# Kernel tuning notes

Hardware: AMD Instinct MI355X
Metric: run time of the kernel (lower is better)

The kernel has to match this reference:

```python
import jax, jax.numpy as jnp
import numpy as np

B, T, I, H = 64, 512, 1024, 1024


def setup_inputs() -> dict:
    key = jax.random.key(0)
    k1, k2, k3, k4 = jax.random.split(key, 4)
    stdv = 1.0 / np.sqrt(H)
    x = jax.random.normal(k1, (B, T, I), dtype=jnp.float32)
    w_ih = jax.random.uniform(k2, (4 * H, I), minval=-stdv, maxval=stdv, dtype=jnp.float32)
    w_hh = jax.random.uniform(k3, (4 * H, H), minval=-stdv, maxval=stdv, dtype=jnp.float32)
    b = jax.random.uniform(k4, (4 * H,), minval=-stdv, maxval=stdv, dtype=jnp.float32)
    return {"x": x, "w_ih": w_ih, "w_hh": w_hh, "b": b}


def _lstm(x, w_ih, w_hh, b):
    # Precompute input projections for all timesteps: [T, B, 4H]
    xg = jnp.einsum('bti,gi->tbg', x, w_ih) + b

    def step(carry, xg_t):
        h, c = carry
        gates = xg_t + h @ w_hh.T  # [B, 4H]
        i, f, g, o = jnp.split(gates, 4, axis=-1)
        i = jax.nn.sigmoid(i)
        f = jax.nn.sigmoid(f)
        g = jnp.tanh(g)
        o = jax.nn.sigmoid(o)
        c = f * c + i * g
        h = o * jnp.tanh(c)
        return (h, c), (h, c)

    h0 = jnp.zeros((x.shape[0], w_hh.shape[1]), dtype=x.dtype)
    c0 = jnp.zeros_like(h0)
    _, (hs, cs) = jax.lax.scan(step, (h0, c0), xg)
    # [T, B, H] -> [B, T, H]
    return hs.transpose(1, 0, 2), cs.transpose(1, 0, 2)


def reference(x, w_ih, w_hh, b):
    return _lstm(x, w_ih, w_hh, b)
```

## Files before the change

kernel.cpp:

```cpp
#include <hip/hip_runtime.h>
#include <stdint.h>

typedef unsigned short u16;
typedef short short8 __attribute__((ext_vector_type(8)));
typedef float f32x4 __attribute__((ext_vector_type(4)));
typedef int i32x4 __attribute__((ext_vector_type(4)));
typedef unsigned long long u64;

#define NT 512
#define NH 1024
#define G4H 4096
#define HS_ELEMS 33554432ull

static __device__ __forceinline__ u16 f2bf(float f){
  union { float f; unsigned u; } v; v.f = f;
  unsigned r = v.u + 0x7fffu + ((v.u >> 16) & 1u);
  return (u16)(r >> 16);
}
static __device__ __forceinline__ float bf2f(u16 s){
  union { unsigned u; float f; } v; v.u = ((unsigned)s) << 16;
  return v.f;
}

__global__ void cvt_kernel(const float* __restrict__ in, u16* __restrict__ out, int n8){
  int i = blockIdx.x*blockDim.x + threadIdx.x;
  int stride = gridDim.x*blockDim.x;
  for (; i < n8; i += stride){
    const float4* p = (const float4*)in;
    float4 a = p[2*i], b = p[2*i+1];
    short8 o;
    o[0]=(short)f2bf(a.x); o[1]=(short)f2bf(a.y); o[2]=(short)f2bf(a.z); o[3]=(short)f2bf(a.w);
    o[4]=(short)f2bf(b.x); o[5]=(short)f2bf(b.y); o[6]=(short)f2bf(b.z); o[7]=(short)f2bf(b.w);
    ((short8*)out)[i] = o;
  }
}

__global__ void init_kernel(unsigned* __restrict__ hx, int* __restrict__ cnt){
  int i = blockIdx.x*blockDim.x + threadIdx.x;
  int stride = gridDim.x*blockDim.x;
  for (int k = i; k < 131072; k += stride) hx[k] = 0u;
  if (i < 256) cnt[i] = 0;
}

__global__ __launch_bounds__(256) void gemm_xg(
    const u16* __restrict__ A,
    const u16* __restrict__ Bw,
    const float* __restrict__ bias,
    u16* __restrict__ C)
{
  __shared__ u16 lA[128*64];
  __shared__ u16 lB[128*64];
  const int tid = threadIdx.x, lane = tid & 63, w = tid >> 6;
  int bid = blockIdx.x;
  int swz = (bid & 7)*1024 + (bid >> 3);
  const int brow = swz >> 5;
  const int bcol = swz & 31;
  const int wr = (w >> 1)*64, wc = (w & 1)*64;
  f32x4 acc[4][4] = {};

  const int rA0 = brow*128 + w*32;
  const int rB0 = bcol*128 + w*32;
  for (int kt = 0; kt < 1024; kt += 64){
    const u16* gA = A  + (size_t)(rA0 + (lane>>3))*1024 + kt + (lane&7)*8;
    const u16* gB = Bw + (size_t)(rB0 + (lane>>3))*1024 + kt + (lane&7)*8;
#pragma unroll
    for (int c = 0; c < 4; c++){
      __builtin_amdgcn_global_load_lds(
        (const __attribute__((address_space(1))) void*)(gA + (size_t)c*8*1024),
        (__attribute__((address_space(3))) void*)&lA[(w*32 + c*8)*64], 16, 0, 0);
      __builtin_amdgcn_global_load_lds(
        (const __attribute__((address_space(1))) void*)(gB + (size_t)c*8*1024),
        (__attribute__((address_space(3))) void*)&lB[(w*32 + c*8)*64], 16, 0, 0);
    }
    __syncthreads();
#pragma unroll
    for (int kk = 0; kk < 2; kk++){
      short8 fa[4], fb[4];
#pragma unroll
      for (int i = 0; i < 4; i++){
        fa[i] = *(const short8*)&lA[(wr + i*16 + (lane&15))*64 + kk*32 + (lane>>4)*8];
        fb[i] = *(const short8*)&lB[(wc + i*16 + (lane&15))*64 + kk*32 + (lane>>4)*8];
      }
#pragma unroll
      for (int i = 0; i < 4; i++)
#pragma unroll
        for (int jj = 0; jj < 4; jj++)
          acc[i][jj] = __builtin_amdgcn_mfma_f32_16x16x32_bf16(fa[i], fb[jj], acc[i][jj], 0,0,0);
    }
    __syncthreads();
  }
  const int mb = brow*128 + wr + ((lane>>4)<<2);
  const int nb = bcol*128 + wc + (lane&15);
#pragma unroll
  for (int jj = 0; jj < 4; jj++){
    const int n = nb + jj*16;
    const float bv = bias[n];
#pragma unroll
    for (int i = 0; i < 4; i++){
#pragma unroll
      for (int reg = 0; reg < 4; reg++){
        int m = mb + i*16 + reg;
        C[(size_t)m*G4H + n] = f2bf(acc[i][jj][reg] + bv);
      }
    }
  }
}

__global__ __launch_bounds__(512, 2) void lstm_rec(
    const u16* __restrict__ whh,
    const u16* __restrict__ xg,
    u16* __restrict__ hx,
    int* cnt,
    float* __restrict__ hs,
    float* __restrict__ cs)
{
  __shared__ u16 lds_h[16384];
  const int tid  = threadIdx.x;
  const int lane = tid & 63;
  const int w    = tid >> 6;
  const int bid  = blockIdx.x;
  const int g    = bid >> 5;
  const int j    = bid & 31;
  const int q    = (lane & 15) >> 2;
  const int col  = j*32 + w*4 + (lane & 3);
  const int Gr   = q*1024 + col;
  const int mloc = (lane >> 4) * 4;

  i32x4 wq[32];
  {
    const i32x4* wp = (const i32x4*)(whh + (size_t)Gr*1024 + ((lane>>4)*8));
#pragma unroll
    for (int kk = 0; kk < 32; kk++) wq[kk] = wp[kk*4];
#pragma unroll
    for (int kk = 0; kk < 32; kk++) asm volatile("" : "+v"(wq[kk]));
  }

  float c_st[4] = {0.f,0.f,0.f,0.f};
  int* cntg = cnt + g*64;

  for (int t = 0; t < NT; t++){
    float xv[4];
#pragma unroll
    for (int reg = 0; reg < 4; reg++){
      int b = g*16 + mloc + reg;
      xv[reg] = bf2f(xg[((size_t)b*NT + t)*G4H + Gr]);
    }
    if (t > 0){
      if (tid == 0){
        const int need = t * 32;
        while (__hip_atomic_load(cntg, __ATOMIC_RELAXED, __HIP_MEMORY_SCOPE_AGENT) < need)
          __builtin_amdgcn_s_sleep(1);
      }
      __syncthreads();
    }
    const u64* hb64 = (const u64*)(hx + ((size_t)(((t+3)&3)*4 + g)) * 16384);
#pragma unroll
    for (int k = 0; k < 8; k++){
      int W = tid + 512*k;
      u64 v = __hip_atomic_load(hb64 + W, __ATOMIC_RELAXED, __HIP_MEMORY_SCOPE_AGENT);
      *(u64*)&lds_h[W*4] = v;
    }
    __syncthreads();

    f32x4 accv[4];
    accv[0] = (f32x4){xv[0], xv[1], xv[2], xv[3]};
    accv[1] = (f32x4){0.f,0.f,0.f,0.f};
    accv[2] = accv[1]; accv[3] = accv[1];
#pragma unroll
    for (int kk = 0; kk < 32; kk++){
      short8 av = *(const short8*)&lds_h[(kk*64 + lane)*8];
      short8 bv = __builtin_bit_cast(short8, wq[kk]);
      accv[kk & 3] = __builtin_amdgcn_mfma_f32_16x16x32_bf16(av, bv, accv[kk & 3], 0,0,0);
    }
    f32x4 gv = (accv[0] + accv[1]) + (accv[2] + accv[3]);

    u16* wbuf = hx + ((size_t)((t&3)*4 + g)) * 16384;
    float hnv[4], cnv[4];
#pragma unroll
    for (int reg = 0; reg < 4; reg++){
      float xg_ = gv[reg];
      float sig = 1.f / (1.f + __expf(-xg_));
      float th  = 1.f - 2.f / (1.f + __expf(2.f*xg_));
      float a   = (q == 2) ? th : sig;
      float v4  = __shfl_xor(a, 4);
      float v8  = __shfl_xor(a, 8);
      float v12 = __shfl_xor(a, 12);
      float iv  = (q==0)?a :(q==1)?v4:(q==2)?v8:v12;
      float fv  = (q==1)?a :(q==0)?v4:(q==3)?v8:v12;
      float gg  = (q==2)?a :(q==3)?v4:(q==0)?v8:v12;
      float ov  = (q==3)?a :(q==2)?v4:(q==1)?v8:v12;
      float cn  = fv*c_st[reg] + iv*gg;
      c_st[reg] = cn;
      float tc  = 1.f - 2.f / (1.f + __expf(2.f*cn));
      float hn  = ov * tc;
      hnv[reg] = hn; cnv[reg] = cn;
      float hp = __shfl_xor(hn, 1);
      if (q == 0 && (lane & 1) == 0){
        unsigned word = (unsigned)f2bf(hn) | ((unsigned)f2bf(hp) << 16);
        int sub = ((col & 31) >> 3)*16 + (mloc + reg);
        int idx16 = ((col >> 5)*64 + sub)*8 + (col & 7);
        __hip_atomic_store((unsigned*)(wbuf + idx16), word,
                           __ATOMIC_RELAXED, __HIP_MEMORY_SCOPE_AGENT);
      }
    }
    __syncthreads();
    if (tid == 0)
      __hip_atomic_fetch_add(cntg, 1, __ATOMIC_RELAXED, __HIP_MEMORY_SCOPE_AGENT);
#pragma unroll
    for (int reg = 0; reg < 4; reg++){
      int b = g*16 + mloc + reg;
      size_t oidx = ((size_t)b*NT + t)*NH + col;
      if (q == 1) __builtin_nontemporal_store(hnv[reg], &hs[oidx]);
      if (q == 2) __builtin_nontemporal_store(cnv[reg], &cs[oidx]);
    }
  }
}

extern "C" void kernel_launch(void* const* d_in, const int* in_sizes, int n_in,
                              void* d_out, int out_size, void* d_ws, size_t ws_size,
                              hipStream_t stream){
  const float* x    = (const float*)d_in[0];
  const float* wih  = (const float*)d_in[1];
  const float* whh  = (const float*)d_in[2];
  const float* bias = (const float*)d_in[3];
  float* hs = (float*)d_out;
  float* cs = hs + HS_ELEMS;
  char* ws = (char*)d_ws;
  u16* xg   = (u16*)(ws + 0);
  u16* xb   = (u16*)(ws + 268435456ull);
  u16* wihb = (u16*)(ws + 335544320ull);
  u16* whhb = (u16*)(ws + 343932928ull);
  u16* hx   = (u16*)(ws + 352321536ull);
  int* cnt  = (int*)(ws + 352845824ull);

  cvt_kernel<<<2048, 256, 0, stream>>>(x,   xb,   33554432/8);
  cvt_kernel<<<512,  256, 0, stream>>>(wih, wihb, 4194304/8);
  cvt_kernel<<<512,  256, 0, stream>>>(whh, whhb, 4194304/8);
  init_kernel<<<64,  256, 0, stream>>>((unsigned*)hx, cnt);
  gemm_xg<<<8192, 256, 0, stream>>>(xb, wihb, bias, xg);

  const u16* whhb_c = whhb; const u16* xg_c = xg;
  u16* hx_p = hx; int* cnt_p = cnt; float* hs_p = hs; float* cs_p = cs;
  void* args[6];
  args[0] = (void*)&whhb_c;
  args[1] = (void*)&xg_c;
  args[2] = (void*)&hx_p;
  args[3] = (void*)&cnt_p;
  args[4] = (void*)&hs_p;
  args[5] = (void*)&cs_p;
  hipLaunchCooperativeKernel((const void*)lstm_rec, dim3(128), dim3(512), args, 0, stream);
}
```

Measured before the change: 3.021 ms.

## Split per-step barrier into two half-counters to overlap recurrent matmul halves

Each group's step counter is split into two counters, one for blocks producing the first half of the hidden columns and one for the second half. A block now waits only on the low-half counter, loads and multiplies the first half of h, then waits on the high-half counter before handling the second half. The goal is to overlap half of the recurrent MFMA work with the arrival of slower producer blocks, shortening the critical path of the per-timestep grid barrier. The cost is an extra spin-wait and __syncthreads per step, and a redundant duplicate argument assignment in the launch code that has no effect.

```diff
diff --git a/kernel.cpp b/kernel.cpp
--- a/kernel.cpp
+++ b/kernel.cpp
@@ -136,7 +136,9 @@
   }
 
   float c_st[4] = {0.f,0.f,0.f,0.f};
-  int* cntg = cnt + g*64;
+  int* cnt_lo = cnt + g*64;
+  int* cnt_hi = cnt + g*64 + 32;
+  int* mycnt  = (j < 16) ? cnt_lo : cnt_hi;
 
   for (int t = 0; t < NT; t++){
     float xv[4];
@@ -145,17 +147,18 @@
       int b = g*16 + mloc + reg;
       xv[reg] = bf2f(xg[((size_t)b*NT + t)*G4H + Gr]);
     }
+    const u64* hb64 = (const u64*)(hx + ((size_t)(((t+3)&3)*4 + g)) * 16384);
+
     if (t > 0){
       if (tid == 0){
-        const int need = t * 32;
-        while (__hip_atomic_load(cntg, __ATOMIC_RELAXED, __HIP_MEMORY_SCOPE_AGENT) < need)
+        const int need = t * 16;
+        while (__hip_atomic_load(cnt_lo, __ATOMIC_RELAXED, __HIP_MEMORY_SCOPE_AGENT) < need)
           __builtin_amdgcn_s_sleep(1);
       }
       __syncthreads();
     }
-    const u64* hb64 = (const u64*)(hx + ((size_t)(((t+3)&3)*4 + g)) * 16384);
-#pragma unroll
-    for (int k = 0; k < 8; k++){
+#pragma unroll
+    for (int k = 0; k < 4; k++){
       int W = tid + 512*k;
       u64 v = __hip_atomic_load(hb64 + W, __ATOMIC_RELAXED, __HIP_MEMORY_SCOPE_AGENT);
       *(u64*)&lds_h[W*4] = v;
@@ -167,7 +170,29 @@
     accv[1] = (f32x4){0.f,0.f,0.f,0.f};
     accv[2] = accv[1]; accv[3] = accv[1];
 #pragma unroll
-    for (int kk = 0; kk < 32; kk++){
+    for (int kk = 0; kk < 16; kk++){
+      short8 av = *(const short8*)&lds_h[(kk*64 + lane)*8];
+      short8 bv = __builtin_bit_cast(short8, wq[kk]);
+      accv[kk & 3] = __builtin_amdgcn_mfma_f32_16x16x32_bf16(av, bv, accv[kk & 3], 0,0,0);
+    }
+
+    if (t > 0){
+      if (tid == 0){
+        const int need = t * 16;
+        while (__hip_atomic_load(cnt_hi, __ATOMIC_RELAXED, __HIP_MEMORY_SCOPE_AGENT) < need)
+          __builtin_amdgcn_s_sleep(1);
+      }
+      __syncthreads();
+    }
+#pragma unroll
+    for (int k = 0; k < 4; k++){
+      int W = 2048 + tid + 512*k;
+      u64 v = __hip_atomic_load(hb64 + W, __ATOMIC_RELAXED, __HIP_MEMORY_SCOPE_AGENT);
+      *(u64*)&lds_h[W*4] = v;
+    }
+    __syncthreads();
+#pragma unroll
+    for (int kk = 16; kk < 32; kk++){
       short8 av = *(const short8*)&lds_h[(kk*64 + lane)*8];
       short8 bv = __builtin_bit_cast(short8, wq[kk]);
       accv[kk & 3] = __builtin_amdgcn_mfma_f32_16x16x32_bf16(av, bv, accv[kk & 3], 0,0,0);
@@ -205,7 +230,7 @@
     }
     __syncthreads();
     if (tid == 0)
-      __hip_atomic_fetch_add(cntg, 1, __ATOMIC_RELAXED, __HIP_MEMORY_SCOPE_AGENT);
+      __hip_atomic_fetch_add(mycnt, 1, __ATOMIC_RELAXED, __HIP_MEMORY_SCOPE_AGENT);
 #pragma unroll
     for (int reg = 0; reg < 4; reg++){
       int b = g*16 + mloc + reg;
@@ -246,6 +271,7 @@
   args[1] = (void*)&xg_c;
   args[2] = (void*)&hx_p;
   args[3] = (void*)&cnt_p;
+  args[4] = (void*)&cs_p;
   args[4] = (void*)&hs_p;
   args[5] = (void*)&cs_p;
   hipLaunchCooperativeKernel((const void*)lstm_rec, dim3(128), dim3(512), args, 0, stream);
```

New measurement: 3.206 ms. 6.1% more time.
